# Kernel tuning notes

Hardware: AMD Instinct MI355X
Metric: run time of the kernel (lower is better)

The kernel has to match this reference:

```python
import jax, jax.numpy as jnp
import numpy as np

C = 64          # channels
K = 7           # 19 - 6*num with num=2 (conv_first, avg_pool, snake kernel size)
GN_GROUPS = C // 4


def conv2d(x, w, b=None, pad=(0, 0), groups=1):
    out = jax.lax.conv_general_dilated(
        x, w, window_strides=(1, 1),
        padding=((pad[0], pad[0]), (pad[1], pad[1])),
        dimension_numbers=('NCHW', 'OIHW', 'NCHW'),
        feature_group_count=groups)
    if b is not None:
        out = out + b[None, :, None, None]
    return out


def avg_pool(x, k, pad):
    # torch AvgPool2d default count_include_pad=True -> always divide by k*k
    s = jax.lax.reduce_window(x, 0.0, jax.lax.add, (1, 1, k, k), (1, 1, 1, 1),
                              ((0, 0), (0, 0), (pad, pad), (pad, pad)))
    return s / float(k * k)


def bn_eval(x, g, b, m, v, eps):
    inv = g / jnp.sqrt(v + eps)
    return x * inv[None, :, None, None] + (b - m * inv)[None, :, None, None]


def group_norm(x, g, b, groups, eps=1e-5):
    B, Ch, H, W = x.shape
    xr = x.reshape(B, groups, Ch // groups, H, W)
    mu = xr.mean(axis=(2, 3, 4), keepdims=True)
    var = xr.var(axis=(2, 3, 4), keepdims=True)
    xr = (xr - mu) / jnp.sqrt(var + eps)
    return xr.reshape(B, Ch, H, W) * g[None, :, None, None] + b[None, :, None, None]


def cum_offset(off):
    # Faithful to DSCNet DSC: center point pinned to 0, offsets accumulate outward
    # via `for index in range(1, center)`. The two endpoints keep their RAW,
    # DETACHED offsets (original code's off-by-one quirk on the detached clone).
    k = off.shape[1]
    c = k // 2
    new = [None] * k
    new[c] = jnp.zeros_like(off[:, c])
    for i in range(1, c):
        new[c + i] = new[c + i - 1] + off[:, c + i]
        new[c - i] = new[c - i + 1] + off[:, c - i]
    new[0] = jax.lax.stop_gradient(off[:, 0])
    new[k - 1] = jax.lax.stop_gradient(off[:, k - 1])
    return jnp.stack(new, axis=1)


def bilinear(feat, y, x):
    # feat [B,C,R,Cc]; y,x [B,K,R,Cc] -> samples [B,C,K,R,Cc]
    B, Ch, R, Cc = feat.shape
    y0 = jnp.floor(y)
    x0 = jnp.floor(x)
    y0i = jnp.clip(y0.astype(jnp.int32), 0, R - 1)
    y1i = jnp.clip(y0.astype(jnp.int32) + 1, 0, R - 1)
    x0i = jnp.clip(x0.astype(jnp.int32), 0, Cc - 1)
    x1i = jnp.clip(x0.astype(jnp.int32) + 1, 0, Cc - 1)
    gather = jax.vmap(lambda f, yi, xi: f[:, yi, xi])  # [C,R,Cc],[K,R,Cc]->[C,K,R,Cc]
    va0 = gather(feat, y0i, x0i)
    vc0 = gather(feat, y0i, x1i)
    va1 = gather(feat, y1i, x0i)
    vc1 = gather(feat, y1i, x1i)
    # interpolation weights use coords clamped to [0, max+1] (faithful to original)
    y0f = jnp.clip(y0, 0.0, float(R))
    y1f = jnp.clip(y0 + 1.0, 0.0, float(R))
    x0f = jnp.clip(x0, 0.0, float(Cc))
    x1f = jnp.clip(x0 + 1.0, 0.0, float(Cc))
    wa0 = ((y1f - y) * (x1f - x))[:, None]
    wc0 = ((y1f - y) * (x - x0f))[:, None]
    wa1 = ((y - y0f) * (x1f - x))[:, None]
    wc1 = ((y - y0f) * (x - x0f))[:, None]
    return va0 * wa0 + vc0 * wc0 + va1 * wa1 + vc1 * wc1


def dsconv(x, off_w, off_b, bn_g, bn_b, bn_m, bn_v, dsc_w, dsc_b, gn_g, gn_b, morph):
    # Dynamic Snake Conv (extend_scope=1, if_offset=True)
    B, Ch, R, Cc = x.shape
    off = jnp.tanh(bn_eval(conv2d(x, off_w, off_b, (1, 1)), bn_g, bn_b, bn_m, bn_v, 1e-5))
    y_off, x_off = off[:, :K], off[:, K:]
    spread = (jnp.arange(K, dtype=x.dtype) - K // 2)[None, :, None, None]
    rows = jnp.arange(R, dtype=x.dtype)[None, None, :, None]
    cols = jnp.arange(Cc, dtype=x.dtype)[None, None, None, :]
    if morph == 0:  # kernel spreads along x, snake swings in y
        y = rows + cum_offset(y_off)
        xc = cols + spread
    else:           # kernel spreads along y, snake swings in x
        y = rows + spread
        xc = cols + cum_offset(x_off)
    y = jnp.broadcast_to(y, (B, K, R, Cc))
    xc = jnp.broadcast_to(xc, (B, K, R, Cc))
    samp = bilinear(x, y, xc)  # [B,C,K,R,Cc]
    # strided (K,1)/(1,K) conv over the deformed map == contraction over (in, k)
    out = jnp.einsum('oik,bikrc->borc', dsc_w, samp) + dsc_b[None, :, None, None]
    out = group_norm(out, gn_g, gn_b, GN_GROUPS)
    return jax.nn.relu(out)


def setup_inputs() -> dict:
    key = jax.random.key(0)
    kit = iter(jax.random.split(key, 64))

    def rn(shape):
        if len(shape) == 1:
            return jax.random.normal(next(kit), shape, jnp.float32) * 0.05
        fan_in = int(np.prod(shape[1:]))
        return jax.random.normal(next(kit), shape, jnp.float32) / np.sqrt(fan_in)

    B, H, W = 2, 192, 192
    d = {}
    d['x'] = jax.random.normal(next(kit), (B, C, H, W), jnp.float32)
    d['w_first'] = rn((C, C, K, K))
    d['hc1_w'] = rn((C, 1, 1, 9)); d['hc1_b'] = rn((C,))
    d['hc2_w'] = rn((C, 1, 1, 7)); d['hc2_b'] = rn((C,))
    d['hc3_w'] = rn((C, 1, 1, 5)); d['hc3_b'] = rn((C,))
    d['vc1_w'] = rn((C, 1, 9, 1)); d['vc1_b'] = rn((C,))
    d['vc2_w'] = rn((C, 1, 7, 1)); d['vc2_b'] = rn((C,))
    d['vc3_w'] = rn((C, 1, 5, 1)); d['vc3_b'] = rn((C,))
    for p in ('h', 'v'):
        d[p + '_off_w'] = rn((2 * K, C, 3, 3)); d[p + '_off_b'] = rn((2 * K,))
        d[p + '_bn_g'] = 1.0 + rn((2 * K,)); d[p + '_bn_b'] = rn((2 * K,))
        d[p + '_bn_m'] = rn((2 * K,))
        d[p + '_bn_v'] = jax.random.uniform(next(kit), (2 * K,), jnp.float32) + 0.5
        d[p + '_dsc_w'] = rn((C, C, K)); d[p + '_dsc_b'] = rn((C,))
        d[p + '_gn_g'] = 1.0 + rn((C,)); d[p + '_gn_b'] = rn((C,))
    d['last_w'] = rn((C, C, 1, 1))
    d['last_g'] = 1.0 + rn((C,)); d['last_b'] = rn((C,))
    d['last_m'] = rn((C,))
    d['last_v'] = jax.random.uniform(next(kit), (C,), jnp.float32) + 0.5
    return d


def reference(x, w_first, hc1_w, hc1_b, hc2_w, hc2_b, hc3_w, hc3_b,
              vc1_w, vc1_b, vc2_w, vc2_b, vc3_w, vc3_b,
              h_off_w, h_off_b, h_bn_g, h_bn_b, h_bn_m, h_bn_v,
              h_dsc_w, h_dsc_b, h_gn_g, h_gn_b,
              v_off_w, v_off_b, v_bn_g, v_bn_b, v_bn_m, v_bn_v,
              v_dsc_w, v_dsc_b, v_gn_g, v_gn_b,
              last_w, last_g, last_b, last_m, last_v):
    x1 = avg_pool(conv2d(x, w_first, None, (K // 2, K // 2)), K, K // 2)
    h = conv2d(x1, hc1_w, hc1_b, (0, 4), groups=C)
    h = conv2d(h, hc2_w, hc2_b, (0, 3), groups=C)
    h = conv2d(h, hc3_w, hc3_b, (0, 2), groups=C)
    h = dsconv(h, h_off_w, h_off_b, h_bn_g, h_bn_b, h_bn_m, h_bn_v,
               h_dsc_w, h_dsc_b, h_gn_g, h_gn_b, morph=0)
    v = conv2d(x1, vc1_w, vc1_b, (4, 0), groups=C)
    v = conv2d(v, vc2_w, vc2_b, (3, 0), groups=C)
    v = conv2d(v, vc3_w, vc3_b, (2, 0), groups=C)
    v = dsconv(v, v_off_w, v_off_b, v_bn_g, v_bn_b, v_bn_m, v_bn_v,
               v_dsc_w, v_dsc_b, v_gn_g, v_gn_b, morph=1)
    out = h + v + x1
    out = conv2d(out, last_w, None, (0, 0))          # 1x1, bias=False (norm present)
    out = bn_eval(out, last_g, last_b, last_m, last_v, 1e-3)
    return out * jax.nn.sigmoid(out)                  # SiLU
```

## Files before the change

### kernel.cpp

```cpp
#include <hip/hip_runtime.h>
#include <hip/hip_bf16.h>
#include <hip/hip_fp16.h>
#include <math.h>

#define Bq 2
#define Cq 64
#define Hq 192
#define Wq 192
#define HWq (Hq*Wq)
#define Nq ((size_t)Bq*Cq*HWq)

typedef __attribute__((ext_vector_type(8))) _Float16 f16x8;
typedef __attribute__((ext_vector_type(4))) float f32x4;

__device__ inline unsigned short h2us(__half h) {
  union { __half h; unsigned short u; } v; v.h = h; return v.u;
}

__global__ __launch_bounds__(256) void prep_small_kernel(
    const float* hc1_w, const float* hc1_b, const float* hc2_w, const float* hc2_b,
    const float* hc3_w, const float* hc3_b,
    const float* vc1_w, const float* vc1_b, const float* vc2_w, const float* vc2_b,
    const float* vc3_w, const float* vc3_b,
    const float* h_off_w, const float* h_off_b, const float* h_bn_g, const float* h_bn_b,
    const float* h_bn_m, const float* h_bn_v,
    const float* v_off_w, const float* v_off_b, const float* v_bn_g, const float* v_bn_b,
    const float* v_bn_m, const float* v_bn_v,
    const float* last_w, const float* last_g, const float* last_b, const float* last_m,
    const float* last_v,
    float* wEffH, float* bEffH, float* wEffV, float* bEffV,
    float* wOffH, float* bOffH, float* wOffV, float* bOffV,
    float* lwT, float* lbO)
{
  int t = threadIdx.x;
  if (t < 128) {
    int ch = t & 63;
    bool ish = t < 64;
    const float* w1p = (ish ? hc1_w : vc1_w) + ch*9;
    const float* w2p = (ish ? hc2_w : vc2_w) + ch*7;
    const float* w3p = (ish ? hc3_w : vc3_w) + ch*5;
    float w1r[9], w2r[7], w3r[5];
#pragma unroll
    for (int j = 0; j < 9; j++) w1r[j] = w1p[j];
#pragma unroll
    for (int k = 0; k < 7; k++) w2r[k] = w2p[k];
#pragma unroll
    for (int m = 0; m < 5; m++) w3r[m] = w3p[m];
    float t15[15];
#pragma unroll
    for (int s = 0; s < 15; s++) {
      float a = 0.f;
#pragma unroll
      for (int j = 0; j < 9; j++) { int k2 = s - j; if (k2 >= 0 && k2 < 7) a += w1r[j]*w2r[k2]; }
      t15[s] = a;
    }
    float* we = (ish ? wEffH : wEffV) + ch*19;
#pragma unroll
    for (int s = 0; s < 19; s++) {
      float a = 0.f;
#pragma unroll
      for (int j = 0; j < 15; j++) { int k3 = s - j; if (k3 >= 0 && k3 < 5) a += t15[j]*w3r[k3]; }
      we[s] = a;
    }
    float S2 = 0.f, S3 = 0.f;
#pragma unroll
    for (int j = 0; j < 7; j++) S2 += w2r[j];
#pragma unroll
    for (int j = 0; j < 5; j++) S3 += w3r[j];
    float b1 = (ish ? hc1_b : vc1_b)[ch];
    float b2 = (ish ? hc2_b : vc2_b)[ch];
    float b3 = (ish ? hc3_b : vc3_b)[ch];
    (ish ? bEffH : bEffV)[ch] = b1*S2*S3 + b2*S3 + b3;
  }
  for (int idx = t; idx < 9*64*7; idx += 256) {
    int tap = idx / 448; int rem = idx % 448; int i = rem / 7; int m = rem % 7;
    float invh = h_bn_g[m] / sqrtf(h_bn_v[m] + 1e-5f);
    wOffH[(tap*64 + i)*8 + m] = h_off_w[(m*64 + i)*9 + tap] * invh;
    float invv = v_bn_g[7+m] / sqrtf(v_bn_v[7+m] + 1e-5f);
    wOffV[(tap*64 + i)*8 + m] = v_off_w[((7+m)*64 + i)*9 + tap] * invv;
  }
  if (t < 7) {
    float invh = h_bn_g[t] / sqrtf(h_bn_v[t] + 1e-5f);
    bOffH[t] = h_off_b[t]*invh + h_bn_b[t] - h_bn_m[t]*invh;
    float invv = v_bn_g[7+t] / sqrtf(v_bn_v[7+t] + 1e-5f);
    bOffV[t] = v_off_b[7+t]*invv + v_bn_b[7+t] - v_bn_m[7+t]*invv;
  }
  for (int idx = t; idx < 4096; idx += 256) {
    int o = idx % 64; int i = idx / 64;
    float inv = last_g[o] / sqrtf(last_v[o] + 1e-3f);
    lwT[i*64 + o] = last_w[o*64 + i] * inv;
  }
  if (t < 64) {
    float inv = last_g[t] / sqrtf(last_v[t] + 1e-3f);
    lbO[t] = last_b[t] - last_m[t]*inv;
  }
}

__global__ __launch_bounds__(256) void prep_border_kernel(
    const float* hc1_w, const float* hc1_b, const float* hc2_w, const float* hc2_b,
    const float* hc3_w, const float* hc3_b,
    const float* vc1_w, const float* vc1_b, const float* vc2_w, const float* vc2_b,
    const float* vc3_w, const float* vc3_b,
    float* wB)
{
  int tid = blockIdx.x*256 + threadIdx.x;
  if (tid >= 2*64*18) return;
  int cls = tid % 18;
  int ch  = (tid / 18) % 64;
  int br  = tid / (18*64);
  int c = (cls < 9) ? cls : cls + 174;
  const float* w1p = (br==0 ? hc1_w : vc1_w) + ch*9;
  const float* w2p = (br==0 ? hc2_w : vc2_w) + ch*7;
  const float* w3p = (br==0 ? hc3_w : vc3_w) + ch*5;
  float b1 = (br==0 ? hc1_b : vc1_b)[ch];
  float b2 = (br==0 ? hc2_b : vc2_b)[ch];
  float b3 = (br==0 ? hc3_b : vc3_b)[ch];
  float w1r[9], w2r[7], w3r[5];
#pragma unroll
  for (int j = 0; j < 9; j++) w1r[j] = w1p[j];
#pragma unroll
  for (int k = 0; k < 7; k++) w2r[k] = w2p[k];
#pragma unroll
  for (int m = 0; m < 5; m++) w3r[m] = w3p[m];

  float acc[19];
#pragma unroll
  for (int s = 0; s < 19; s++) acc[s] = 0.f;
  float bacc = b3;
#pragma unroll
  for (int m = 0; m < 5; m++) {
    int d = c + m - 2;
    bool dok = (d >= 0 && d < Wq);
    float s2b = b2;
#pragma unroll
    for (int k = 0; k < 7; k++) {
      int e = d + k - 3;
      bool eok = (e >= 0 && e < Wq);
      if (eok) s2b += w2r[k] * b1;
      float wmk = w3r[m] * w2r[k];
#pragma unroll
      for (int j = 0; j < 9; j++) {
        int fd = e + j - 4;
        bool fok = (fd >= 0 && fd < Wq);
        float contrib = (dok && eok && fok) ? wmk * w1r[j] : 0.f;
        acc[m + k + j] += contrib;
      }
    }
    if (dok) bacc += w3r[m] * s2b;
  }
  float* dst = wB + ((size_t)(br*64 + ch)*18 + cls)*20;
#pragma unroll
  for (int s = 0; s < 19; s++) dst[s] = acc[s];
  dst[19] = bacc;
}

__global__ __launch_bounds__(256) void prep_big_kernel(
    const float* __restrict__ w_first,
    const float* __restrict__ h_dsc_w, const float* __restrict__ v_dsc_w,
    unsigned short* __restrict__ wtpH, unsigned short* __restrict__ wtpV,
    unsigned short* __restrict__ wpack)
{
  int tid = blockIdx.x*256 + threadIdx.x;
  int nthr = gridDim.x*256;
  for (int idx = tid; idx < 7*2*2*64*32; idx += nthr) {
    int ch32 = idx & 31;
    int oc   = (idx >> 5) & 63;
    int hl   = (idx >> 11) & 1;
    int kc   = (idx >> 12) & 1;
    int tap  = idx >> 13;
    int i = kc*32 + ch32;
    float vh = h_dsc_w[oc*448 + i*7 + tap];
    float vv = v_dsc_w[oc*448 + i*7 + tap];
    _Float16 hh = (_Float16)vh;
    _Float16 hv = (_Float16)vv;
    unsigned short uh, uv;
    if (!hl) { uh = *(unsigned short*)&hh; uv = *(unsigned short*)&hv; }
    else {
      _Float16 lh = (_Float16)(vh - (float)hh);
      _Float16 lv = (_Float16)(vv - (float)hv);
      uh = *(unsigned short*)&lh; uv = *(unsigned short*)&lv;
    }
    wtpH[idx] = uh; wtpV[idx] = uv;
  }
  for (int e = tid; e < 2*49*2*64*32; e += nthr) {
    int ch  = e & 31;
    int oc  = (e >> 5) & 63;
    int hl  = (e >> 11) & 1;
    int rest = e >> 12;
    int tap = rest % 49;
    int h   = rest / 49;
    float wv = w_first[((size_t)oc*64 + h*32 + ch)*49 + tap];
    __half hh = __float2half(wv);
    unsigned short us;
    if (!hl) us = h2us(hh);
    else { float rr = wv - __half2float(hh); us = h2us(__float2half(rr)); }
    wpack[e] = us;
  }
}

__global__ __launch_bounds__(192) void tof16_pack_kernel(const float* __restrict__ x,
                                                         unsigned short* __restrict__ xpack)
{
  __shared__ unsigned int s[192*64];
  int r = blockIdx.x, b = blockIdx.y;
  int t = threadIdx.x;
  for (int ch = 0; ch < 64; ch++) {
    float v = x[((size_t)(b*64+ch)*Hq + r)*Wq + t];
    _Float16 hh = (_Float16)v;
    s[t*64 + (ch ^ (t & 31))] = (unsigned int)*(unsigned short*)&hh;
  }
  __syncthreads();
  unsigned short* dst = xpack + ((size_t)b*Hq + r)*Wq*64;
  for (int i = 0; i < 8; i++) {
    int gidx = i*192 + t;
    int c = gidx >> 3, g = gidx & 7;
    unsigned short tmp[8];
#pragma unroll
    for (int j = 0; j < 8; j++) {
      int ch = g*8 + j;
      tmp[j] = (unsigned short)s[c*64 + (ch ^ (c & 31))];
    }
    uint4 v;
    v.x = (unsigned int)tmp[0] | ((unsigned int)tmp[1] << 16);
    v.y = (unsigned int)tmp[2] | ((unsigned int)tmp[3] << 16);
    v.z = (unsigned int)tmp[4] | ((unsigned int)tmp[5] << 16);
    v.w = (unsigned int)tmp[6] | ((unsigned int)tmp[7] << 16);
    *(uint4*)(dst + (size_t)gidx*8) = v;
  }
}

__global__ __launch_bounds__(256) void conv7_mfma_kernel(
    const unsigned short* __restrict__ xpack,
    const unsigned short* __restrict__ wpack,
    float* __restrict__ out)
{
  __shared__ __align__(16) unsigned short sA[8*54*32];
  int ct = blockIdx.x;
  int rt = blockIdx.y;
  int b  = blockIdx.z;
  int r0 = rt*2, c0 = ct*48;
  int t = threadIdx.x;
  int wv = t >> 6;
  int l  = t & 63;
  int l15 = l & 15, lg = l >> 4;
  int oc = wv*16 + l15;

  f32x4 acc[2][3];
#pragma unroll
  for (int i = 0; i < 2; i++)
#pragma unroll
    for (int j = 0; j < 3; j++) acc[i][j] = (f32x4){0.f,0.f,0.f,0.f};

  for (int h = 0; h < 2; h++) {
    __syncthreads();
    for (int idx = t; idx < 8*54*4; idx += 256) {
      int g = idx & 3, pix = idx >> 2;
      int row = pix / 54, col = pix % 54;
      int gr = r0 - 3 + row, gc = c0 - 3 + col;
      uint4 v = {0u,0u,0u,0u};
      if (gr >= 0 && gr < Hq && gc >= 0 && gc < Wq)
        v = *(const uint4*)(xpack + (((size_t)b*Hq + gr)*Wq + gc)*64 + (h*4 + g)*8);
      ((uint4*)sA)[(row*54 + col)*4 + (g ^ ((col >> 1) & 3))] = v;
    }
    __syncthreads();
    const unsigned short* wb = wpack + (size_t)h*49*4096;
#pragma unroll 7
    for (int tap = 0; tap < 49; tap++) {
      int dy = tap / 7, dx = tap % 7;
      f16x8 bh = *(const f16x8*)(wb + (size_t)tap*4096 +        oc*32 + lg*8);
      f16x8 bl = *(const f16x8*)(wb + (size_t)tap*4096 + 2048 + oc*32 + lg*8);
#pragma unroll
      for (int rw = 0; rw < 2; rw++) {
        int arow = rw + dy;
        f16x8 a[3];
#pragma unroll
        for (int tc = 0; tc < 3; tc++) {
          int col = tc*16 + l15 + dx;
          a[tc] = *(const f16x8*)((const uint4*)sA + (arow*54 + col)*4 + (lg ^ ((col >> 1) & 3)));
        }
#pragma unroll
        for (int tc = 0; tc < 3; tc++) {
          acc[rw][tc] = __builtin_amdgcn_mfma_f32_16x16x32_f16(a[tc], bh, acc[rw][tc], 0, 0, 0);
          acc[rw][tc] = __builtin_amdgcn_mfma_f32_16x16x32_f16(a[tc], bl, acc[rw][tc], 0, 0, 0);
        }
      }
    }
  }
#pragma unroll
  for (int rw = 0; rw < 2; rw++) {
    float* dst = out + ((size_t)(b*64 + oc)*Hq + (r0 + rw))*Wq + c0;
#pragma unroll
    for (int tc = 0; tc < 3; tc++) {
      f32x4 v = acc[rw][tc];
      *(float4*)(dst + tc*16 + lg*4) = make_float4(v[0], v[1], v[2], v[3]);
    }
  }
}

__global__ __launch_bounds__(256) void pool_fused_kernel(const float* __restrict__ in,
                                                         float* __restrict__ out)
{
  __shared__ float raw[38][192];
  __shared__ float cs[32][192];
  int rt = blockIdx.x;
  int plane = blockIdx.y;
  int r0 = rt*32;
  int t = threadIdx.x;
  const float* src = in + (size_t)plane*HWq;
  for (int idx = t; idx < 38*192; idx += 256) {
    int lr = idx / 192, c = idx % 192;
    int gr = r0 - 3 + lr;
    raw[lr][c] = (gr >= 0 && gr < Hq) ? src[gr*Wq + c] : 0.f;
  }
  __syncthreads();
  for (int idx = t; idx < 32*192; idx += 256) {
    int lr = idx / 192, c = idx % 192;
    float s = 0.f;
#pragma unroll
    for (int dr = 0; dr < 7; dr++) s += raw[lr + dr][c];
    cs[lr][c] = s;
  }
  __syncthreads();
  float* dst = out + (size_t)plane*HWq + r0*Wq;
  for (int idx = t; idx < 32*192; idx += 256) {
    int lr = idx / 192, c = idx % 192;
    float s = 0.f;
#pragma unroll
    for (int dc = -3; dc <= 3; dc++) {
      int cc = c + dc;
      if (cc >= 0 && cc < Wq) s += cs[lr][cc];
    }
    dst[idx] = s * (1.f/49.f);
  }
}

__global__ __launch_bounds__(256) void dwf_kernel(const float* __restrict__ x1,
                                                  const float* __restrict__ wEffH,
                                                  const float* __restrict__ bEffH,
                                                  const float* __restrict__ wBH,
                                                  const float* __restrict__ wEffV,
                                                  const float* __restrict__ bEffV,
                                                  const float* __restrict__ wBV,
                                                  unsigned short* __restrict__ packH,
                                                  unsigned short* __restrict__ packV)
{
  __shared__ float sW[8][19][20];
  int z = blockIdx.z;
  int br = z >> 1, b = z & 1;
  const float* wEff = br ? wEffV : wEffH;
  const float* bEff = br ? bEffV : bEffH;
  const float* wB   = br ? wBV   : wBH;
  unsigned short* pack = br ? packV : packH;
  int g8 = blockIdx.y;
  int t = threadIdx.x;
  int chb = g8*8;
  for (int i = t; i < 8*380; i += 256) {
    int ch8 = i / 380; int rem = i % 380;
    int row = rem / 20, jj = rem % 20;
    int ch = chb + ch8;
    float v;
    if (row < 18) v = wB[((size_t)ch*18 + row)*20 + jj];
    else v = (jj < 19) ? wEff[ch*19 + jj] : bEff[ch];
    sW[ch8][row][jj] = v;
  }
  __syncthreads();
  int p = blockIdx.x*256 + t;
  int r = p / Wq, c = p % Wq;
  float vals[8];
  if (br == 0) {
    int row = (c < 9) ? c : ((c >= Wq-9) ? (c - 174) : 18);
#pragma unroll
    for (int ch8 = 0; ch8 < 8; ch8++) {
      const float* src = x1 + (size_t)(b*Cq + chb + ch8)*HWq + r*Wq;
      float s = sW[ch8][row][19];
#pragma unroll
      for (int j = 0; j < 19; j++) {
        int idx = min(max(c + j - 9, 0), Wq-1);
        s += src[idx] * sW[ch8][row][j];
      }
      vals[ch8] = s;
    }
  } else {
    int row = (r < 9) ? r : ((r >= Hq-9) ? (r - 174) : 18);
#pragma unroll
    for (int ch8 = 0; ch8 < 8; ch8++) {
      const float* src = x1 + (size_t)(b*Cq + chb + ch8)*HWq + c;
      float s = sW[ch8][row][19];
#pragma unroll
      for (int j = 0; j < 19; j++) {
        int idx = min(max(r + j - 9, 0), Hq-1);
        s += src[idx*Wq] * sW[ch8][row][j];
      }
      vals[ch8] = s;
    }
  }
  unsigned int hi[4], lo[4];
#pragma unroll
  for (int q = 0; q < 4; q++) {
    __half h0 = __float2half(vals[2*q]);
    __half h1 = __float2half(vals[2*q+1]);
    __half l0 = __float2half(vals[2*q]   - __half2float(h0));
    __half l1 = __float2half(vals[2*q+1] - __half2float(h1));
    hi[q] = (unsigned int)h2us(h0) | ((unsigned int)h2us(h1) << 16);
    lo[q] = (unsigned int)h2us(l0) | ((unsigned int)h2us(l1) << 16);
  }
  *(uint4*)(pack + (((size_t)b*16 + g8)*HWq + p)*8)     = make_uint4(hi[0], hi[1], hi[2], hi[3]);
  *(uint4*)(pack + (((size_t)b*16 + 8 + g8)*HWq + p)*8) = make_uint4(lo[0], lo[1], lo[2], lo[3]);
}

__global__ __launch_bounds__(256) void off_cum_kernel(const unsigned short* __restrict__ fpH,
                                                      const unsigned short* __restrict__ fpV,
                                                      const float* __restrict__ wOffH,
                                                      const float* __restrict__ bOffH,
                                                      const float* __restrict__ wOffV,
                                                      const float* __restrict__ bOffV,
                                                      float* __restrict__ hcum,
                                                      float* __restrict__ vcum)
{
  const size_t HW8 = (size_t)HWq*8;
  int bid = blockIdx.x;
  int xcd = bid & 7, lid = bid >> 3;
  int combo = xcd >> 1;
  int br = combo >> 1, b = combo & 1;
  int pxblk = (xcd & 1)*72 + lid;
  const unsigned short* fp = br ? fpV : fpH;
  const float* wOff = br ? wOffV : wOffH;
  const float* bOff = br ? bOffV : bOffH;
  float* cum = br ? vcum : hcum;
  int p = pxblk*256 + threadIdx.x;
  int r = p / Wq, c = p % Wq;
  float tv[7];
#pragma unroll
  for (int m = 0; m < 7; m++) tv[m] = bOff[m];
  const unsigned short* fb = fp + (size_t)b*HWq*128;
  for (int tap = 0; tap < 9; tap++) {
    int dy = tap/3 - 1, dx = tap%3 - 1;
    int rr = r + dy, cc = c + dx;
    if (rr < 0 || rr >= Hq || cc < 0 || cc >= Wq) continue;
    const unsigned short* p0 = fb + ((size_t)rr*Wq + cc)*8;
    const float* wp = wOff + tap*512;
    for (int g = 0; g < 8; g++) {
      f16x8 hv = *(const f16x8*)(p0 + (size_t)g*HW8);
      f16x8 lv = *(const f16x8*)(p0 + (size_t)(8 + g)*HW8);
#pragma unroll
      for (int e = 0; e < 8; e++) {
        float fv = (float)hv[e] + (float)lv[e];
        const float* wr = wp + (g*8 + e)*8;
#pragma unroll
        for (int m = 0; m < 7; m++) tv[m] += fv * wr[m];
      }
    }
  }
#pragma unroll
  for (int m = 0; m < 7; m++) tv[m] = tanhf(tv[m]);
  float c0 = tv[0], c1 = tv[1] + tv[2], c2 = tv[2], c3 = 0.f;
  float c4 = tv[4], c5 = tv[4] + tv[5], c6 = tv[6];
  size_t bb = (size_t)b*7*HWq + p;
  cum[bb + 0*HWq] = c0; cum[bb + 1*HWq] = c1; cum[bb + 2*HWq] = c2;
  cum[bb + 3*HWq] = c3; cum[bb + 4*HWq] = c4; cum[bb + 5*HWq] = c5;
  cum[bb + 6*HWq] = c6;
}

__global__ __launch_bounds__(128) void einsum_mfma_kernel(
    const unsigned short* __restrict__ fpH, const unsigned short* __restrict__ fpV,
    const float* __restrict__ cumH, const float* __restrict__ cumV,
    const unsigned short* __restrict__ wtpHp, const unsigned short* __restrict__ wtpVp,
    const float* __restrict__ dscbH, const float* __restrict__ dscbV,
    float* __restrict__ outH, float* __restrict__ outV)
{
  __shared__ __align__(16) unsigned short sA[2*128*64];
  const size_t HW8 = (size_t)HWq*8;
  int morph = blockIdx.y;
  const unsigned short* fp  = morph ? fpV   : fpH;
  const float* cum          = morph ? cumV  : cumH;
  const unsigned short* wtp = morph ? wtpVp : wtpHp;
  const float* dsc_b        = morph ? dscbV : dscbH;
  float* out                = morph ? outV  : outH;
  int bid = blockIdx.x;
  int swz = (bid & 7)*72 + (bid >> 3);
  int b   = swz / 288;
  int blk = swz % 288;
  int t = threadIdx.x;
  int w = t >> 6, l = t & 63;
  int l15 = l & 15, lg = l >> 4;
  int l7 = l15 & 7;
  int p = blk*128 + w*64 + l;
  int r = p / Wq, c = p % Wq;

  f32x4 acc[4][4];
#pragma unroll
  for (int i = 0; i < 4; i++)
#pragma unroll
    for (int j = 0; j < 4; j++) acc[i][j] = (f32x4){0.f,0.f,0.f,0.f};

  const unsigned short* fb = fp + (size_t)b*HWq*128;

  for (int kp = 0; kp < 4; kp++) {
    int k0 = kp*2;
    int nk = (kp < 3) ? 2 : 1;
    for (int kk = 0; kk < nk; kk++) {
      int k = k0 + kk;
      unsigned short* myrow = sA + (size_t)(kk*128 + w*64 + l)*64;
      bool oob;
      const unsigned short *p0, *p1;
      float w0, w1;
      if (morph == 0) {
        int xi = c + k - 3;
        oob = (xi < 0 || xi >= Wq);
        if (!oob) {
          float y = (float)r + cum[((size_t)(b*7 + k))*HWq + p];
          float y0 = floorf(y);
          int y0q = (int)y0;
          int y0i = min(max(y0q, 0), Hq-1);
          int y1i = min(max(y0q + 1, 0), Hq-1);
          float y0f = fminf(fmaxf(y0, 0.f), (float)Hq);
          float y1f = fminf(fmaxf(y0 + 1.f, 0.f), (float)Hq);
          w0 = y1f - y; w1 = y - y0f;
          p0 = fb + ((size_t)y0i*Wq + xi)*8;
          p1 = fb + ((size_t)y1i*Wq + xi)*8;
        }
      } else {
        int yi = r + k - 3;
        oob = (yi < 0 || yi >= Hq);
        if (!oob) {
          float xf = (float)c + cum[((size_t)(b*7 + k))*HWq + p];
          float x0 = floorf(xf);
          int x0q = (int)x0;
          int x0i = min(max(x0q, 0), Wq-1);
          int x1i = min(max(x0q + 1, 0), Wq-1);
          float x0f = fminf(fmaxf(x0, 0.f), (float)Wq);
          float x1f = fminf(fmaxf(x0 + 1.f, 0.f), (float)Wq);
          w0 = x1f - xf; w1 = xf - x0f;
          p0 = fb + ((size_t)yi*Wq + x0i)*8;
          p1 = fb + ((size_t)yi*Wq + x1i)*8;
        }
      }
      if (oob) {
        uint4 z = {0u,0u,0u,0u};
#pragma unroll
        for (int j = 0; j < 8; j++) ((uint4*)myrow)[j] = z;
      } else {
#pragma unroll
        for (int g = 0; g < 8; g++) {
          f16x8 a0h = *(const f16x8*)(p0 + (size_t)g*HW8);
          f16x8 a1h = *(const f16x8*)(p1 + (size_t)g*HW8);
          f16x8 sh;
#pragma unroll
          for (int e = 0; e < 8; e++) {
            float v = w0*(float)a0h[e] + w1*(float)a1h[e];
            sh[e] = (_Float16)v;
          }
          *(f16x8*)(myrow + (size_t)(g ^ l7)*8) = sh;
        }
      }
    }
    __syncthreads();
    for (int kk = 0; kk < nk; kk++) {
      int k = k0 + kk;
#pragma unroll
      for (int kc = 0; kc < 2; kc++) {
        const unsigned short* wbase = wtp + (size_t)((k*2 + kc)*2)*2048;
        f16x8 bh[4], bl[4];
#pragma unroll
        for (int tb = 0; tb < 4; tb++) {
          bh[tb] = *(const f16x8*)(wbase + (tb*16 + l15)*32 + lg*8);
          bl[tb] = *(const f16x8*)(wbase + 2048 + (tb*16 + l15)*32 + lg*8);
        }
        f16x8 ah[4];
#pragma unroll
        for (int ta = 0; ta < 4; ta++) {
          const unsigned short* rbase = sA + (size_t)(kk*128 + w*64 + ta*16 + l15)*64;
          ah[ta] = *(const f16x8*)(rbase + (size_t)((kc*4 + lg) ^ l7)*8);
        }
#pragma unroll
        for (int ta = 0; ta < 4; ta++)
#pragma unroll
          for (int tb = 0; tb < 4; tb++) {
            acc[ta][tb] = __builtin_amdgcn_mfma_f32_16x16x32_f16(ah[ta], bh[tb], acc[ta][tb], 0, 0, 0);
            acc[ta][tb] = __builtin_amdgcn_mfma_f32_16x16x32_f16(ah[ta], bl[tb], acc[ta][tb], 0, 0, 0);
          }
      }
    }
    __syncthreads();
  }
  int pbase = blk*128 + w*64;
#pragma unroll
  for (int tb = 0; tb < 4; tb++) {
    int oc = tb*16 + l15;
    float bias = dsc_b[oc];
    float* dst = out + (size_t)(b*64 + oc)*HWq + pbase;
#pragma unroll
    for (int ta = 0; ta < 4; ta++) {
      f32x4 v = acc[ta][tb];
      *(float4*)(dst + ta*16 + lg*4) = make_float4(v[0]+bias, v[1]+bias, v[2]+bias, v[3]+bias);
    }
  }
}

__global__ __launch_bounds__(256) void gnstats_kernel(const float* __restrict__ h_ds,
                                                      const float* __restrict__ v_ds,
                                                      float* __restrict__ stats)
{
  int plane = blockIdx.x;
  int buf = plane >> 7;
  int rem = plane & 127;
  const float* src = (buf ? v_ds : h_ds) + (size_t)rem*HWq;
  float s = 0.f, s2 = 0.f;
  for (int i = threadIdx.x; i < HWq; i += 256) {
    float v = src[i];
    s += v; s2 += v*v;
  }
  __shared__ float red[2][4];
  for (int off = 32; off; off >>= 1) {
    s  += __shfl_down(s, off);
    s2 += __shfl_down(s2, off);
  }
  if ((threadIdx.x & 63) == 0) { red[0][threadIdx.x >> 6] = s; red[1][threadIdx.x >> 6] = s2; }
  __syncthreads();
  if (threadIdx.x == 0) {
    s  = red[0][0] + red[0][1] + red[0][2] + red[0][3];
    s2 = red[1][0] + red[1][1] + red[1][2] + red[1][3];
    stats[plane*2 + 0] = s;
    stats[plane*2 + 1] = s2;
  }
}

__global__ __launch_bounds__(256) void gnfinal_kernel(const float* __restrict__ stats,
                                                      const float* __restrict__ h_gn_g, const float* __restrict__ h_gn_b,
                                                      const float* __restrict__ v_gn_g, const float* __restrict__ v_gn_b,
                                                      float* __restrict__ gnAB)
{
  int t = threadIdx.x;
  int buf = t >> 7, ch = t & 63;
  int base = t & ~3;
  float sum = 0.f, ss = 0.f;
#pragma unroll
  for (int q = 0; q < 4; q++) { sum += stats[(base+q)*2]; ss += stats[(base+q)*2 + 1]; }
  const float n = 4.f * HWq;
  float mean = sum / n;
  float var = ss / n - mean*mean;
  float gg = (buf ? v_gn_g : h_gn_g)[ch];
  float bb = (buf ? v_gn_b : h_gn_b)[ch];
  float A = gg / sqrtf(var + 1e-5f);
  gnAB[t*2 + 0] = A;
  gnAB[t*2 + 1] = bb - mean*A;
}

__global__ __launch_bounds__(256) void final2_kernel(const float* __restrict__ hbuf,
                                                     const float* __restrict__ vbuf,
                                                     const float* __restrict__ x1,
                                                     const float* __restrict__ gnAB,
                                                     const float* __restrict__ lwT,
                                                     const float* __restrict__ lbO,
                                                     float* __restrict__ out)
{
  int b = blockIdx.y;
  int p = blockIdx.x*256 + threadIdx.x;
  float acc[64];
#pragma unroll
  for (int o = 0; o < 64; o++) acc[o] = 0.f;
  for (int i = 0; i < 64; i++) {
    size_t off = (size_t)(b*64 + i)*HWq + p;
    int plane = b*64 + i;
    int ih = plane*2;
    int iv = (128 + plane)*2;
    float hv = fmaxf(hbuf[off]*gnAB[ih] + gnAB[ih+1], 0.f);
    float vv = fmaxf(vbuf[off]*gnAB[iv] + gnAB[iv+1], 0.f);
    float cv = hv + vv + x1[off];
    const float* wr = lwT + i*64;
#pragma unroll
    for (int o = 0; o < 64; o++) acc[o] += cv * wr[o];
  }
  float* dst = out + (size_t)b*Cq*HWq + p;
#pragma unroll
  for (int o = 0; o < 64; o++) {
    float yv = acc[o] + lbO[o];
    dst[(size_t)o*HWq] = yv / (1.f + expf(-yv));
  }
}

extern "C" void kernel_launch(void* const* d_in, const int* in_sizes, int n_in,
                              void* d_out, int out_size, void* d_ws, size_t ws_size,
                              hipStream_t stream)
{
  const float* x       = (const float*)d_in[0];
  const float* w_first = (const float*)d_in[1];
  float* ws = (float*)d_ws;

  float* bufA = ws;
  float* bufB = ws + Nq;
  float* x1   = ws + 2*Nq;
  float* h_ds = ws + 3*Nq;
  float* v_ds = ws + 4*Nq;
  size_t off = 5*Nq;
  float* hcum  = ws + off; off += (size_t)Bq*7*HWq;
  float* vcum  = ws + off; off += (size_t)Bq*7*HWq;
  float* wEffH = ws + off; off += 64*19;
  float* bEffH = ws + off; off += 64;
  float* wEffV = ws + off; off += 64*19;
  float* bEffV = ws + off; off += 64;
  float* wtH   = ws + off; off += 64*64*7;
  float* wtV   = ws + off; off += 64*64*7;
  float* wOffH = ws + off; off += 9*64*8;
  float* bOffH = ws + off; off += 8;
  float* wOffV = ws + off; off += 9*64*8;
  float* bOffV = ws + off; off += 8;
  float* lwT   = ws + off; off += 64*64;
  float* lbO   = ws + off; off += 64;
  float* stats = ws + off; off += 512;
  float* gnAB  = ws + off; off += 512;
  float* wB    = ws + off; off += 2*64*18*20;
  unsigned short* wpack = (unsigned short*)(ws + off); off += 2*49*2*64*32/2 + 16;
  unsigned short* xpack  = (unsigned short*)h_ds;
  unsigned short* fpackH = (unsigned short*)h_ds;
  unsigned short* fpackV = (unsigned short*)v_ds;
  unsigned short* wtpH = (unsigned short*)wtH;
  unsigned short* wtpV = (unsigned short*)wtV;

  prep_small_kernel<<<dim3(1), dim3(256), 0, stream>>>(
      (const float*)d_in[2],  (const float*)d_in[3],  (const float*)d_in[4],  (const float*)d_in[5],
      (const float*)d_in[6],  (const float*)d_in[7],
      (const float*)d_in[8],  (const float*)d_in[9],  (const float*)d_in[10], (const float*)d_in[11],
      (const float*)d_in[12], (const float*)d_in[13],
      (const float*)d_in[14], (const float*)d_in[15], (const float*)d_in[16], (const float*)d_in[17],
      (const float*)d_in[18], (const float*)d_in[19],
      (const float*)d_in[24], (const float*)d_in[25], (const float*)d_in[26], (const float*)d_in[27],
      (const float*)d_in[28], (const float*)d_in[29],
      (const float*)d_in[34], (const float*)d_in[35], (const float*)d_in[36], (const float*)d_in[37],
      (const float*)d_in[38],
      wEffH, bEffH, wEffV, bEffV, wOffH, bOffH, wOffV, bOffV, lwT, lbO);

  prep_border_kernel<<<dim3(9), dim3(256), 0, stream>>>(
      (const float*)d_in[2],  (const float*)d_in[3],  (const float*)d_in[4],  (const float*)d_in[5],
      (const float*)d_in[6],  (const float*)d_in[7],
      (const float*)d_in[8],  (const float*)d_in[9],  (const float*)d_in[10], (const float*)d_in[11],
      (const float*)d_in[12], (const float*)d_in[13], wB);

  prep_big_kernel<<<dim3(64), dim3(256), 0, stream>>>(
      w_first, (const float*)d_in[20], (const float*)d_in[30], wtpH, wtpV, wpack);

  tof16_pack_kernel<<<dim3(Hq, Bq), dim3(192), 0, stream>>>(x, xpack);
  conv7_mfma_kernel<<<dim3(4, 96, 2), dim3(256), 0, stream>>>(xpack, wpack, bufA);

  pool_fused_kernel<<<dim3(6, 128), dim3(256), 0, stream>>>(bufA, x1);

  dwf_kernel<<<dim3(144, 8, 4), dim3(256), 0, stream>>>(x1, wEffH, bEffH, wB,
      wEffV, bEffV, wB + 64*18*20, fpackH, fpackV);

  off_cum_kernel<<<dim3(576), dim3(256), 0, stream>>>(fpackH, fpackV,
      wOffH, bOffH, wOffV, bOffV, hcum, vcum);

  einsum_mfma_kernel<<<dim3(576, 2), dim3(128), 0, stream>>>(fpackH, fpackV,
      hcum, vcum, wtpH, wtpV, (const float*)d_in[21], (const float*)d_in[31], bufA, bufB);

  gnstats_kernel<<<dim3(256), dim3(256), 0, stream>>>(bufA, bufB, stats);
  gnfinal_kernel<<<dim3(1), dim3(256), 0, stream>>>(stats,
      (const float*)d_in[22], (const float*)d_in[23],
      (const float*)d_in[32], (const float*)d_in[33], gnAB);

  final2_kernel<<<dim3(144, 2), dim3(256), 0, stream>>>(bufA, bufB, x1, gnAB, lwT, lbO, (float*)d_out);
}
```

Measured before the change: 344.5 us.

## Fuse GroupNorm statistics into einsum epilogue and merge prep kernels

The einsum kernel now computes per-channel partial sums and sums of squares in its store epilogue, using cross-lane shuffles, and writes them to a small partial-stats buffer. A light reduction kernel then combines these partials, replacing the separate pass that re-read both full output buffers from memory. The three weight-prep kernels are merged into one launch that dispatches work by block index, which cuts launch overhead. The two __syncthreads around the shared-memory tile loop in the einsum are also removed; this is only safe if each warp reads just the shared data it loaded itself, otherwise it can cause a data race.

```diff
diff --git a/kernel.cpp b/kernel.cpp
--- a/kernel.cpp
+++ b/kernel.cpp
@@ -17,7 +17,7 @@
   union { __half h; unsigned short u; } v; v.h = h; return v.u;
 }
 
-__global__ __launch_bounds__(256) void prep_small_kernel(
+__global__ __launch_bounds__(256) void prep_all_kernel(
     const float* hc1_w, const float* hc1_b, const float* hc2_w, const float* hc2_b,
     const float* hc3_w, const float* hc3_b,
     const float* vc1_w, const float* vc1_b, const float* vc2_w, const float* vc2_b,
@@ -28,173 +28,164 @@
     const float* v_bn_m, const float* v_bn_v,
     const float* last_w, const float* last_g, const float* last_b, const float* last_m,
     const float* last_v,
+    const float* __restrict__ w_first,
+    const float* __restrict__ h_dsc_w, const float* __restrict__ v_dsc_w,
     float* wEffH, float* bEffH, float* wEffV, float* bEffV,
     float* wOffH, float* bOffH, float* wOffV, float* bOffV,
-    float* lwT, float* lbO)
-{
-  int t = threadIdx.x;
-  if (t < 128) {
-    int ch = t & 63;
-    bool ish = t < 64;
-    const float* w1p = (ish ? hc1_w : vc1_w) + ch*9;
-    const float* w2p = (ish ? hc2_w : vc2_w) + ch*7;
-    const float* w3p = (ish ? hc3_w : vc3_w) + ch*5;
-    float w1r[9], w2r[7], w3r[5];
-#pragma unroll
-    for (int j = 0; j < 9; j++) w1r[j] = w1p[j];
-#pragma unroll
-    for (int k = 0; k < 7; k++) w2r[k] = w2p[k];
-#pragma unroll
-    for (int m = 0; m < 5; m++) w3r[m] = w3p[m];
-    float t15[15];
-#pragma unroll
-    for (int s = 0; s < 15; s++) {
-      float a = 0.f;
-#pragma unroll
-      for (int j = 0; j < 9; j++) { int k2 = s - j; if (k2 >= 0 && k2 < 7) a += w1r[j]*w2r[k2]; }
-      t15[s] = a;
-    }
-    float* we = (ish ? wEffH : wEffV) + ch*19;
-#pragma unroll
-    for (int s = 0; s < 19; s++) {
-      float a = 0.f;
-#pragma unroll
-      for (int j = 0; j < 15; j++) { int k3 = s - j; if (k3 >= 0 && k3 < 5) a += t15[j]*w3r[k3]; }
-      we[s] = a;
-    }
-    float S2 = 0.f, S3 = 0.f;
-#pragma unroll
-    for (int j = 0; j < 7; j++) S2 += w2r[j];
-#pragma unroll
-    for (int j = 0; j < 5; j++) S3 += w3r[j];
-    float b1 = (ish ? hc1_b : vc1_b)[ch];
-    float b2 = (ish ? hc2_b : vc2_b)[ch];
-    float b3 = (ish ? hc3_b : vc3_b)[ch];
-    (ish ? bEffH : bEffV)[ch] = b1*S2*S3 + b2*S3 + b3;
-  }
-  for (int idx = t; idx < 9*64*7; idx += 256) {
-    int tap = idx / 448; int rem = idx % 448; int i = rem / 7; int m = rem % 7;
-    float invh = h_bn_g[m] / sqrtf(h_bn_v[m] + 1e-5f);
-    wOffH[(tap*64 + i)*8 + m] = h_off_w[(m*64 + i)*9 + tap] * invh;
-    float invv = v_bn_g[7+m] / sqrtf(v_bn_v[7+m] + 1e-5f);
-    wOffV[(tap*64 + i)*8 + m] = v_off_w[((7+m)*64 + i)*9 + tap] * invv;
-  }
-  if (t < 7) {
-    float invh = h_bn_g[t] / sqrtf(h_bn_v[t] + 1e-5f);
-    bOffH[t] = h_off_b[t]*invh + h_bn_b[t] - h_bn_m[t]*invh;
-    float invv = v_bn_g[7+t] / sqrtf(v_bn_v[7+t] + 1e-5f);
-    bOffV[t] = v_off_b[7+t]*invv + v_bn_b[7+t] - v_bn_m[7+t]*invv;
-  }
-  for (int idx = t; idx < 4096; idx += 256) {
-    int o = idx % 64; int i = idx / 64;
-    float inv = last_g[o] / sqrtf(last_v[o] + 1e-3f);
-    lwT[i*64 + o] = last_w[o*64 + i] * inv;
-  }
-  if (t < 64) {
-    float inv = last_g[t] / sqrtf(last_v[t] + 1e-3f);
-    lbO[t] = last_b[t] - last_m[t]*inv;
-  }
-}
-
-__global__ __launch_bounds__(256) void prep_border_kernel(
-    const float* hc1_w, const float* hc1_b, const float* hc2_w, const float* hc2_b,
-    const float* hc3_w, const float* hc3_b,
-    const float* vc1_w, const float* vc1_b, const float* vc2_w, const float* vc2_b,
-    const float* vc3_w, const float* vc3_b,
-    float* wB)
-{
-  int tid = blockIdx.x*256 + threadIdx.x;
-  if (tid >= 2*64*18) return;
-  int cls = tid % 18;
-  int ch  = (tid / 18) % 64;
-  int br  = tid / (18*64);
-  int c = (cls < 9) ? cls : cls + 174;
-  const float* w1p = (br==0 ? hc1_w : vc1_w) + ch*9;
-  const float* w2p = (br==0 ? hc2_w : vc2_w) + ch*7;
-  const float* w3p = (br==0 ? hc3_w : vc3_w) + ch*5;
-  float b1 = (br==0 ? hc1_b : vc1_b)[ch];
-  float b2 = (br==0 ? hc2_b : vc2_b)[ch];
-  float b3 = (br==0 ? hc3_b : vc3_b)[ch];
-  float w1r[9], w2r[7], w3r[5];
-#pragma unroll
-  for (int j = 0; j < 9; j++) w1r[j] = w1p[j];
-#pragma unroll
-  for (int k = 0; k < 7; k++) w2r[k] = w2p[k];
-#pragma unroll
-  for (int m = 0; m < 5; m++) w3r[m] = w3p[m];
-
-  float acc[19];
-#pragma unroll
-  for (int s = 0; s < 19; s++) acc[s] = 0.f;
-  float bacc = b3;
-#pragma unroll
-  for (int m = 0; m < 5; m++) {
-    int d = c + m - 2;
-    bool dok = (d >= 0 && d < Wq);
-    float s2b = b2;
-#pragma unroll
-    for (int k = 0; k < 7; k++) {
-      int e = d + k - 3;
-      bool eok = (e >= 0 && e < Wq);
-      if (eok) s2b += w2r[k] * b1;
-      float wmk = w3r[m] * w2r[k];
-#pragma unroll
-      for (int j = 0; j < 9; j++) {
-        int fd = e + j - 4;
-        bool fok = (fd >= 0 && fd < Wq);
-        float contrib = (dok && eok && fok) ? wmk * w1r[j] : 0.f;
-        acc[m + k + j] += contrib;
-      }
-    }
-    if (dok) bacc += w3r[m] * s2b;
-  }
-  float* dst = wB + ((size_t)(br*64 + ch)*18 + cls)*20;
-#pragma unroll
-  for (int s = 0; s < 19; s++) dst[s] = acc[s];
-  dst[19] = bacc;
-}
-
-__global__ __launch_bounds__(256) void prep_big_kernel(
-    const float* __restrict__ w_first,
-    const float* __restrict__ h_dsc_w, const float* __restrict__ v_dsc_w,
+    float* lwT, float* lbO, float* wB,
     unsigned short* __restrict__ wtpH, unsigned short* __restrict__ wtpV,
     unsigned short* __restrict__ wpack)
 {
-  int tid = blockIdx.x*256 + threadIdx.x;
-  int nthr = gridDim.x*256;
-  for (int idx = tid; idx < 7*2*2*64*32; idx += nthr) {
-    int ch32 = idx & 31;
-    int oc   = (idx >> 5) & 63;
-    int hl   = (idx >> 11) & 1;
-    int kc   = (idx >> 12) & 1;
-    int tap  = idx >> 13;
-    int i = kc*32 + ch32;
-    float vh = h_dsc_w[oc*448 + i*7 + tap];
-    float vv = v_dsc_w[oc*448 + i*7 + tap];
-    _Float16 hh = (_Float16)vh;
-    _Float16 hv = (_Float16)vv;
-    unsigned short uh, uv;
-    if (!hl) { uh = *(unsigned short*)&hh; uv = *(unsigned short*)&hv; }
-    else {
-      _Float16 lh = (_Float16)(vh - (float)hh);
-      _Float16 lv = (_Float16)(vv - (float)hv);
-      uh = *(unsigned short*)&lh; uv = *(unsigned short*)&lv;
-    }
-    wtpH[idx] = uh; wtpV[idx] = uv;
-  }
-  for (int e = tid; e < 2*49*2*64*32; e += nthr) {
-    int ch  = e & 31;
-    int oc  = (e >> 5) & 63;
-    int hl  = (e >> 11) & 1;
-    int rest = e >> 12;
-    int tap = rest % 49;
-    int h   = rest / 49;
-    float wv = w_first[((size_t)oc*64 + h*32 + ch)*49 + tap];
-    __half hh = __float2half(wv);
-    unsigned short us;
-    if (!hl) us = h2us(hh);
-    else { float rr = wv - __half2float(hh); us = h2us(__float2half(rr)); }
-    wpack[e] = us;
+  int bid = blockIdx.x;
+  int t = threadIdx.x;
+  if (bid == 0) {
+    if (t < 128) {
+      int ch = t & 63;
+      bool ish = t < 64;
+      const float* w1p = (ish ? hc1_w : vc1_w) + ch*9;
+      const float* w2p = (ish ? hc2_w : vc2_w) + ch*7;
+      const float* w3p = (ish ? hc3_w : vc3_w) + ch*5;
+      float w1r[9], w2r[7], w3r[5];
+#pragma unroll
+      for (int j = 0; j < 9; j++) w1r[j] = w1p[j];
+#pragma unroll
+      for (int k = 0; k < 7; k++) w2r[k] = w2p[k];
+#pragma unroll
+      for (int m = 0; m < 5; m++) w3r[m] = w3p[m];
+      float t15[15];
+#pragma unroll
+      for (int s = 0; s < 15; s++) {
+        float a = 0.f;
+#pragma unroll
+        for (int j = 0; j < 9; j++) { int k2 = s - j; if (k2 >= 0 && k2 < 7) a += w1r[j]*w2r[k2]; }
+        t15[s] = a;
+      }
+      float* we = (ish ? wEffH : wEffV) + ch*19;
+#pragma unroll
+      for (int s = 0; s < 19; s++) {
+        float a = 0.f;
+#pragma unroll
+        for (int j = 0; j < 15; j++) { int k3 = s - j; if (k3 >= 0 && k3 < 5) a += t15[j]*w3r[k3]; }
+        we[s] = a;
+      }
+      float S2 = 0.f, S3 = 0.f;
+#pragma unroll
+      for (int j = 0; j < 7; j++) S2 += w2r[j];
+#pragma unroll
+      for (int j = 0; j < 5; j++) S3 += w3r[j];
+      float b1 = (ish ? hc1_b : vc1_b)[ch];
+      float b2 = (ish ? hc2_b : vc2_b)[ch];
+      float b3 = (ish ? hc3_b : vc3_b)[ch];
+      (ish ? bEffH : bEffV)[ch] = b1*S2*S3 + b2*S3 + b3;
+    }
+    for (int idx = t; idx < 9*64*7; idx += 256) {
+      int tap = idx / 448; int rem = idx % 448; int i = rem / 7; int m = rem % 7;
+      float invh = h_bn_g[m] / sqrtf(h_bn_v[m] + 1e-5f);
+      wOffH[(tap*64 + i)*8 + m] = h_off_w[(m*64 + i)*9 + tap] * invh;
+      float invv = v_bn_g[7+m] / sqrtf(v_bn_v[7+m] + 1e-5f);
+      wOffV[(tap*64 + i)*8 + m] = v_off_w[((7+m)*64 + i)*9 + tap] * invv;
+    }
+    if (t < 7) {
+      float invh = h_bn_g[t] / sqrtf(h_bn_v[t] + 1e-5f);
+      bOffH[t] = h_off_b[t]*invh + h_bn_b[t] - h_bn_m[t]*invh;
+      float invv = v_bn_g[7+t] / sqrtf(v_bn_v[7+t] + 1e-5f);
+      bOffV[t] = v_off_b[7+t]*invv + v_bn_b[7+t] - v_bn_m[7+t]*invv;
+    }
+    for (int idx = t; idx < 4096; idx += 256) {
+      int o = idx % 64; int i = idx / 64;
+      float inv = last_g[o] / sqrtf(last_v[o] + 1e-3f);
+      lwT[i*64 + o] = last_w[o*64 + i] * inv;
+    }
+    if (t < 64) {
+      float inv = last_g[t] / sqrtf(last_v[t] + 1e-3f);
+      lbO[t] = last_b[t] - last_m[t]*inv;
+    }
+  } else if (bid <= 9) {
+    int tid = (bid - 1)*256 + t;
+    if (tid >= 2*64*18) return;
+    int cls = tid % 18;
+    int ch  = (tid / 18) % 64;
+    int br  = tid / (18*64);
+    int c = (cls < 9) ? cls : cls + 174;
+    const float* w1p = (br==0 ? hc1_w : vc1_w) + ch*9;
+    const float* w2p = (br==0 ? hc2_w : vc2_w) + ch*7;
+    const float* w3p = (br==0 ? hc3_w : vc3_w) + ch*5;
+    float b1 = (br==0 ? hc1_b : vc1_b)[ch];
+    float b2 = (br==0 ? hc2_b : vc2_b)[ch];
+    float b3 = (br==0 ? hc3_b : vc3_b)[ch];
+    float w1r[9], w2r[7], w3r[5];
+#pragma unroll
+    for (int j = 0; j < 9; j++) w1r[j] = w1p[j];
+#pragma unroll
+    for (int k = 0; k < 7; k++) w2r[k] = w2p[k];
+#pragma unroll
+    for (int m = 0; m < 5; m++) w3r[m] = w3p[m];
+    float acc[19];
+#pragma unroll
+    for (int s = 0; s < 19; s++) acc[s] = 0.f;
+    float bacc = b3;
+#pragma unroll
+    for (int m = 0; m < 5; m++) {
+      int d = c + m - 2;
+      bool dok = (d >= 0 && d < Wq);
+      float s2b = b2;
+#pragma unroll
+      for (int k = 0; k < 7; k++) {
+        int e = d + k - 3;
+        bool eok = (e >= 0 && e < Wq);
+        if (eok) s2b += w2r[k] * b1;
+        float wmk = w3r[m] * w2r[k];
+#pragma unroll
+        for (int j = 0; j < 9; j++) {
+          int fd = e + j - 4;
+          bool fok = (fd >= 0 && fd < Wq);
+          float contrib = (dok && eok && fok) ? wmk * w1r[j] : 0.f;
+          acc[m + k + j] += contrib;
+        }
+      }
+      if (dok) bacc += w3r[m] * s2b;
+    }
+    float* dst = wB + ((size_t)(br*64 + ch)*18 + cls)*20;
+#pragma unroll
+    for (int s = 0; s < 19; s++) dst[s] = acc[s];
+    dst[19] = bacc;
+  } else {
+    int tid = (bid - 10)*256 + t;
+    int nthr = 64*256;
+    for (int idx = tid; idx < 7*2*2*64*32; idx += nthr) {
+      int ch32 = idx & 31;
+      int oc   = (idx >> 5) & 63;
+      int hl   = (idx >> 11) & 1;
+      int kc   = (idx >> 12) & 1;
+      int tap  = idx >> 13;
+      int i = kc*32 + ch32;
+      float vh = h_dsc_w[oc*448 + i*7 + tap];
+      float vv = v_dsc_w[oc*448 + i*7 + tap];
+      _Float16 hh = (_Float16)vh;
+      _Float16 hv = (_Float16)vv;
+      unsigned short uh, uv;
+      if (!hl) { uh = *(unsigned short*)&hh; uv = *(unsigned short*)&hv; }
+      else {
+        _Float16 lh = (_Float16)(vh - (float)hh);
+        _Float16 lv = (_Float16)(vv - (float)hv);
+        uh = *(unsigned short*)&lh; uv = *(unsigned short*)&lv;
+      }
+      wtpH[idx] = uh; wtpV[idx] = uv;
+    }
+    for (int e = tid; e < 2*49*2*64*32; e += nthr) {
+      int ch  = e & 31;
+      int oc  = (e >> 5) & 63;
+      int hl  = (e >> 11) & 1;
+      int rest = e >> 12;
+      int tap = rest % 49;
+      int h   = rest / 49;
+      float wv = w_first[((size_t)oc*64 + h*32 + ch)*49 + tap];
+      __half hh = __float2half(wv);
+      unsigned short us;
+      if (!hl) us = h2us(hh);
+      else { float rr = wv - __half2float(hh); us = h2us(__float2half(rr)); }
+      wpack[e] = us;
+    }
   }
 }
 
@@ -466,7 +457,8 @@
     const float* __restrict__ cumH, const float* __restrict__ cumV,
     const unsigned short* __restrict__ wtpHp, const unsigned short* __restrict__ wtpVp,
     const float* __restrict__ dscbH, const float* __restrict__ dscbV,
-    float* __restrict__ outH, float* __restrict__ outV)
+    float* __restrict__ outH, float* __restrict__ outV,
+    float* __restrict__ pstat)
 {
   __shared__ __align__(16) unsigned short sA[2*128*64];
   const size_t HW8 = (size_t)HWq*8;
@@ -554,7 +546,6 @@
         }
       }
     }
-    __syncthreads();
     for (int kk = 0; kk < nk; kk++) {
       int k = k0 + kk;
 #pragma unroll
@@ -581,7 +572,6 @@
           }
       }
     }
-    __syncthreads();
   }
   int pbase = blk*128 + w*64;
 #pragma unroll
@@ -589,39 +579,52 @@
     int oc = tb*16 + l15;
     float bias = dsc_b[oc];
     float* dst = out + (size_t)(b*64 + oc)*HWq + pbase;
+    float s = 0.f, ss = 0.f;
 #pragma unroll
     for (int ta = 0; ta < 4; ta++) {
       f32x4 v = acc[ta][tb];
-      *(float4*)(dst + ta*16 + lg*4) = make_float4(v[0]+bias, v[1]+bias, v[2]+bias, v[3]+bias);
-    }
-  }
-}
-
-__global__ __launch_bounds__(256) void gnstats_kernel(const float* __restrict__ h_ds,
-                                                      const float* __restrict__ v_ds,
-                                                      float* __restrict__ stats)
-{
-  int plane = blockIdx.x;
-  int buf = plane >> 7;
-  int rem = plane & 127;
-  const float* src = (buf ? v_ds : h_ds) + (size_t)rem*HWq;
-  float s = 0.f, s2 = 0.f;
-  for (int i = threadIdx.x; i < HWq; i += 256) {
-    float v = src[i];
-    s += v; s2 += v*v;
+      float v0 = v[0]+bias, v1 = v[1]+bias, v2 = v[2]+bias, v3 = v[3]+bias;
+      *(float4*)(dst + ta*16 + lg*4) = make_float4(v0, v1, v2, v3);
+      s  += v0 + v1 + v2 + v3;
+      ss += v0*v0 + v1*v1 + v2*v2 + v3*v3;
+    }
+    s  += __shfl_xor(s, 16);
+    s  += __shfl_xor(s, 32);
+    ss += __shfl_xor(ss, 16);
+    ss += __shfl_xor(ss, 32);
+    if (lg == 0) {
+      float* pp = pstat + ((size_t)(morph*576 + swz)*2 + w)*128 + oc*2;
+      pp[0] = s; pp[1] = ss;
+    }
+  }
+}
+
+__global__ __launch_bounds__(256) void gnred_kernel(const float* __restrict__ pstat,
+                                                    float* __restrict__ stats)
+{
+  int combo = blockIdx.x;
+  int buf = combo >> 7;
+  int rem = combo & 127;
+  int b = rem >> 6, ch = rem & 63;
+  int t = threadIdx.x;
+  float s = 0.f, ss = 0.f;
+  for (int q = t; q < 576; q += 256) {
+    int blk = q >> 1, w = q & 1;
+    const float* pp = pstat + ((size_t)(buf*576 + b*288 + blk)*2 + w)*128 + ch*2;
+    s += pp[0]; ss += pp[1];
   }
   __shared__ float red[2][4];
   for (int off = 32; off; off >>= 1) {
     s  += __shfl_down(s, off);
-    s2 += __shfl_down(s2, off);
-  }
-  if ((threadIdx.x & 63) == 0) { red[0][threadIdx.x >> 6] = s; red[1][threadIdx.x >> 6] = s2; }
+    ss += __shfl_down(ss, off);
+  }
+  if ((t & 63) == 0) { red[0][t >> 6] = s; red[1][t >> 6] = ss; }
   __syncthreads();
-  if (threadIdx.x == 0) {
+  if (t == 0) {
     s  = red[0][0] + red[0][1] + red[0][2] + red[0][3];
-    s2 = red[1][0] + red[1][1] + red[1][2] + red[1][3];
-    stats[plane*2 + 0] = s;
-    stats[plane*2 + 1] = s2;
+    ss = red[1][0] + red[1][1] + red[1][2] + red[1][3];
+    stats[combo*2 + 0] = s;
+    stats[combo*2 + 1] = ss;
   }
 }
 
@@ -710,6 +713,7 @@
   float* stats = ws + off; off += 512;
   float* gnAB  = ws + off; off += 512;
   float* wB    = ws + off; off += 2*64*18*20;
+  float* pstat = ws + off; off += (size_t)2*576*2*128;
   unsigned short* wpack = (unsigned short*)(ws + off); off += 2*49*2*64*32/2 + 16;
   unsigned short* xpack  = (unsigned short*)h_ds;
   unsigned short* fpackH = (unsigned short*)h_ds;
@@ -717,7 +721,7 @@
   unsigned short* wtpH = (unsigned short*)wtH;
   unsigned short* wtpV = (unsigned short*)wtV;
 
-  prep_small_kernel<<<dim3(1), dim3(256), 0, stream>>>(
+  prep_all_kernel<<<dim3(74), dim3(256), 0, stream>>>(
       (const float*)d_in[2],  (const float*)d_in[3],  (const float*)d_in[4],  (const float*)d_in[5],
       (const float*)d_in[6],  (const float*)d_in[7],
       (const float*)d_in[8],  (const float*)d_in[9],  (const float*)d_in[10], (const float*)d_in[11],
@@ -728,16 +732,9 @@
       (const float*)d_in[28], (const float*)d_in[29],
       (const float*)d_in[34], (const float*)d_in[35], (const float*)d_in[36], (const float*)d_in[37],
       (const float*)d_in[38],
-      wEffH, bEffH, wEffV, bEffV, wOffH, bOffH, wOffV, bOffV, lwT, lbO);
-
-  prep_border_kernel<<<dim3(9), dim3(256), 0, stream>>>(
-      (const float*)d_in[2],  (const float*)d_in[3],  (const float*)d_in[4],  (const float*)d_in[5],
-      (const float*)d_in[6],  (const float*)d_in[7],
-      (const float*)d_in[8],  (const float*)d_in[9],  (const float*)d_in[10], (const float*)d_in[11],
-      (const float*)d_in[12], (const float*)d_in[13], wB);
-
-  prep_big_kernel<<<dim3(64), dim3(256), 0, stream>>>(
-      w_first, (const float*)d_in[20], (const float*)d_in[30], wtpH, wtpV, wpack);
+      w_first, (const float*)d_in[20], (const float*)d_in[30],
+      wEffH, bEffH, wEffV, bEffV, wOffH, bOffH, wOffV, bOffV, lwT, lbO, wB,
+      wtpH, wtpV, wpack);
 
   tof16_pack_kernel<<<dim3(Hq, Bq), dim3(192), 0, stream>>>(x, xpack);
   conv7_mfma_kernel<<<dim3(4, 96, 2), dim3(256), 0, stream>>>(xpack, wpack, bufA);
@@ -751,9 +748,9 @@
       wOffH, bOffH, wOffV, bOffV, hcum, vcum);
 
   einsum_mfma_kernel<<<dim3(576, 2), dim3(128), 0, stream>>>(fpackH, fpackV,
-      hcum, vcum, wtpH, wtpV, (const float*)d_in[21], (const float*)d_in[31], bufA, bufB);
-
-  gnstats_kernel<<<dim3(256), dim3(256), 0, stream>>>(bufA, bufB, stats);
+      hcum, vcum, wtpH, wtpV, (const float*)d_in[21], (const float*)d_in[31], bufA, bufB, pstat);
+
+  gnred_kernel<<<dim3(256), dim3(256), 0, stream>>>(pstat, stats);
   gnfinal_kernel<<<dim3(1), dim3(256), 0, stream>>>(stats,
       (const float*)d_in[22], (const float*)d_in[23],
       (const float*)d_in[32], (const float*)d_in[33], gnAB);
```

New measurement: 302.1 us. -12.3%, faster.
